# Kernel optimization log

Hardware: AMD Instinct MI355X
Metric: run time of the kernel (lower is better)

Reference implementation:

```python
import jax, jax.numpy as jnp
import numpy as np

D_MODEL = 1024
N_HEADS = 16
D_FF = 512  # FeedForward default d_ff=512 (not overridden in EncoderLayer)
EPS = 1e-6


def _norm(x, alpha, bias):
    # Custom NormLayer: mean + UNBIASED variance (torch.var default, N-1 denom)
    mean = jnp.mean(x, axis=-1, keepdims=True)
    n = x.shape[-1]
    var = jnp.sum((x - mean) ** 2, axis=-1, keepdims=True) / (n - 1)
    return alpha * (x - mean) / jnp.sqrt(var + EPS) + bias


def setup_inputs() -> dict:
    key = jax.random.key(0)
    ks = jax.random.split(key, 12)
    s = 1.0 / np.sqrt(D_MODEL)
    inp = {
        "x": jax.random.normal(ks[0], (2, 2048, D_MODEL), dtype=jnp.float32),
        "Wq": jax.random.uniform(ks[1], (D_MODEL, D_MODEL), jnp.float32, -s, s),
        "bq": jnp.zeros((D_MODEL,), jnp.float32),
        "Wk": jax.random.uniform(ks[2], (D_MODEL, D_MODEL), jnp.float32, -s, s),
        "bk": jnp.zeros((D_MODEL,), jnp.float32),
        "Wv": jax.random.uniform(ks[3], (D_MODEL, D_MODEL), jnp.float32, -s, s),
        "bv": jnp.zeros((D_MODEL,), jnp.float32),
        "Wo": jax.random.uniform(ks[4], (D_MODEL, D_MODEL), jnp.float32, -s, s),
        "bo": jnp.zeros((D_MODEL,), jnp.float32),
        "alpha1": jnp.ones((D_MODEL,), jnp.float32),
        "beta1": jnp.zeros((D_MODEL,), jnp.float32),
        "alpha2": jnp.ones((D_MODEL,), jnp.float32),
        "beta2": jnp.zeros((D_MODEL,), jnp.float32),
        "W1": jax.random.uniform(ks[5], (D_MODEL, D_FF), jnp.float32, -s, s),
        "b1": jnp.zeros((D_FF,), jnp.float32),
        "W2": jax.random.uniform(ks[6], (D_FF, D_MODEL), jnp.float32, -1.0 / np.sqrt(D_FF), 1.0 / np.sqrt(D_FF)),
        "b2": jnp.zeros((D_MODEL,), jnp.float32),
    }
    return inp


def reference(x, Wq, bq, Wk, bk, Wv, bv, Wo, bo, alpha1, beta1, alpha2, beta2, W1, b1, W2, b2):
    B, S, D = x.shape
    H = N_HEADS
    dh = D // H
    # norm_1 applied to x, result feeds BOTH attention and the residual
    x = _norm(x, alpha1, beta1)
    # multihead attention (dropout = identity in eval)
    q = (x @ Wq + bq).reshape(B, S, H, dh)
    k = (x @ Wk + bk).reshape(B, S, H, dh)
    v = (x @ Wv + bv).reshape(B, S, H, dh)
    scores = jnp.einsum("bqhd,bkhd->bhqk", q, k) / jnp.sqrt(jnp.asarray(dh, x.dtype))
    attn = jax.nn.softmax(scores, axis=-1)
    o = jnp.einsum("bhqk,bkhd->bqhd", attn, v).reshape(B, S, D)
    o = o @ Wo + bo
    x = x + o
    # FFN on norm_2(x)
    h = _norm(x, alpha2, beta2)
    h = jax.nn.relu(h @ W1 + b1) @ W2 + b2
    return x + h
```

## Files before the change

kernel.cpp:

```cpp
#include <hip/hip_runtime.h>

typedef __bf16 bf16;
typedef __bf16 bf16x4 __attribute__((ext_vector_type(4)));
typedef __bf16 bf16x8 __attribute__((ext_vector_type(8)));
typedef float f32x4 __attribute__((ext_vector_type(4)));

#define D_MODEL 1024
#define SEQ 2048
#define NB 2
#define LOG2E 1.4426950408889634f

__device__ __forceinline__ void glds16(const bf16* g, bf16* l) {
    __builtin_amdgcn_global_load_lds(
        (const __attribute__((address_space(1))) void*)g,
        (__attribute__((address_space(3))) void*)l, 16, 0, 0);
}

__device__ __forceinline__ void tile_tcvt(
    const float* __restrict__ src, int rows, int cols, bf16* __restrict__ dst,
    int bx, int by, bf16 (*t)[72])
{
    int tid = threadIdx.x;
    int k0 = by * 64, n0 = bx * 64;
    int r = tid >> 2, c = (tid & 3) * 16;
    const float4* s = (const float4*)(src + (size_t)(k0 + r) * cols + n0 + c);
#pragma unroll
    for (int q = 0; q < 4; ++q) {
        float4 v = s[q];
        t[c + q * 4 + 0][r] = (bf16)v.x;
        t[c + q * 4 + 1][r] = (bf16)v.y;
        t[c + q * 4 + 2][r] = (bf16)v.z;
        t[c + q * 4 + 3][r] = (bf16)v.w;
    }
    __syncthreads();
    bf16* d = dst + (size_t)(n0 + r) * rows + k0 + c;
    *(bf16x8*)(d)     = *(const bf16x8*)&t[r][c];
    *(bf16x8*)(d + 8) = *(const bf16x8*)&t[r][c + 8];
}

__device__ __forceinline__ void norm_row(
    const float* __restrict__ X, const float* __restrict__ alpha,
    const float* __restrict__ beta, bf16* __restrict__ Y, int row)
{
    int tid = threadIdx.x;
    float4 v = ((const float4*)(X + (size_t)row * D_MODEL))[tid];
    float s = v.x + v.y + v.z + v.w;
    float ss = v.x*v.x + v.y*v.y + v.z*v.z + v.w*v.w;
#pragma unroll
    for (int off = 1; off < 64; off <<= 1) {
        s  += __shfl_xor(s, off, 64);
        ss += __shfl_xor(ss, off, 64);
    }
    __shared__ float sd[8];
    int wave = tid >> 6, lane = tid & 63;
    if (lane == 0) { sd[wave] = s; sd[4 + wave] = ss; }
    __syncthreads();
    s  = sd[0] + sd[1] + sd[2] + sd[3];
    ss = sd[4] + sd[5] + sd[6] + sd[7];
    float mean = s * (1.0f / 1024.0f);
    float var  = (ss - s * mean) * (1.0f / 1023.0f);
    float rs = rsqrtf(var + 1e-6f);
    float4 a = ((const float4*)alpha)[tid];
    float4 bt = ((const float4*)beta)[tid];
    bf16x4 o;
    o[0] = (bf16)(a.x * (v.x - mean) * rs + bt.x);
    o[1] = (bf16)(a.y * (v.y - mean) * rs + bt.y);
    o[2] = (bf16)(a.z * (v.z - mean) * rs + bt.z);
    o[3] = (bf16)(a.w * (v.w - mean) * rs + bt.w);
    *(bf16x4*)(Y + (size_t)row * D_MODEL + tid * 4) = o;
}

__global__ __launch_bounds__(256) void prep_norm_kernel(
    const float* __restrict__ x, const float* __restrict__ alpha1,
    const float* __restrict__ beta1, bf16* __restrict__ xn,
    const float* __restrict__ Wq, const float* __restrict__ Wk,
    const float* __restrict__ Wv, const float* __restrict__ Wo,
    const float* __restrict__ W1, const float* __restrict__ W2,
    const float* __restrict__ bq, const float* __restrict__ bk,
    const float* __restrict__ bv,
    bf16* __restrict__ Wqkv_t, bf16* __restrict__ Wo_t,
    bf16* __restrict__ W1_t, bf16* __restrict__ W2_t,
    float* __restrict__ b_qkv)
{
    __shared__ bf16 t[64][72];
    int id = blockIdx.x;
    if (id < 4096) {
        norm_row(x, alpha1, beta1, xn, id);
        return;
    }
    id -= 4096;
    if (id < 1024) {
        int which = id >> 8, tile = id & 255;
        const float* src = which == 0 ? Wq : which == 1 ? Wk : which == 2 ? Wv : Wo;
        bf16* dst = which == 3 ? Wo_t : Wqkv_t + (size_t)which * 1024 * 1024;
        tile_tcvt(src, 1024, 1024, dst, tile & 15, tile >> 4, t);
    } else if (id < 1152) {
        int tile = id - 1024;
        tile_tcvt(W1, 1024, 512, W1_t, tile & 7, tile >> 3, t);
    } else if (id < 1280) {
        int tile = id - 1152;
        tile_tcvt(W2, 512, 1024, W2_t, tile & 15, tile >> 4, t);
    } else {
        int i = (id - 1280) * 256 + threadIdx.x;
        float v;
        if (i < 1024) v = bq[i];
        else if (i < 2048) v = bk[i - 1024];
        else v = bv[i - 2048];
        b_qkv[i] = v;
    }
}

__global__ __launch_bounds__(256) void norm_kernel(
    const float* __restrict__ X, const float* __restrict__ alpha,
    const float* __restrict__ beta, bf16* __restrict__ Y)
{
    norm_row(X, alpha, beta, Y, blockIdx.x);
}

__global__ __launch_bounds__(256) void crelu_kernel(
    const float* __restrict__ p0, const float* __restrict__ p1,
    const float* __restrict__ b1, bf16* __restrict__ h1)
{
    int i = blockIdx.x * 256 + threadIdx.x;
    float4 a = ((const float4*)p0)[i];
    float4 b = ((const float4*)p1)[i];
    int col = (i * 4) & 511;
    float4 bb = *(const float4*)(b1 + col);
    bf16x4 o;
    o[0] = (bf16)fmaxf(a.x + b.x + bb.x, 0.0f);
    o[1] = (bf16)fmaxf(a.y + b.y + bb.y, 0.0f);
    o[2] = (bf16)fmaxf(a.z + b.z + bb.z, 0.0f);
    o[3] = (bf16)fmaxf(a.w + b.w + bb.w, 0.0f);
    ((bf16x4*)h1)[i] = o;
}

template <typename OutT, int BN, int KU, bool VFUSE, bool SPLITK>
__global__ __launch_bounds__(256) void gemm128(
    const bf16* __restrict__ A, const bf16* __restrict__ Bt,
    const float* __restrict__ bias, const bf16* __restrict__ Rb,
    const float* __restrict__ Rf, OutT* __restrict__ C, bf16* __restrict__ vT,
    int M, int N, int K, int lda, int relu)
{
    constexpr int NT = BN / 32;
    constexpr int ASTR = 128 * 32;
    constexpr int BSTR = BN * 32;
    __shared__ bf16 As[ASTR * KU];
    __shared__ bf16 Bs[BSTR * KU];

    int tid = threadIdx.x;
    int wave = tid >> 6, lane = tid & 63;
    int quad = lane >> 4, l16 = lane & 15;
    int m0 = blockIdx.y * 128, n0 = blockIdx.x * BN;
    int wm = (wave >> 1) * 64, wn = (wave & 1) * (BN / 2);
    int Keff = SPLITK ? (K >> 1) : K;
    int klo  = SPLITK ? blockIdx.z * Keff : 0;

    f32x4 acc[4][NT] = {};

    const bf16* ga = A  + (size_t)(m0 + (tid >> 2)) * lda + (tid & 3) * 8 + klo;
    const bf16* gb = Bt + (size_t)(n0 + (tid >> 2)) * K   + (tid & 3) * 8 + klo;
    bf16* lAs = As + wave * 512;
    bf16* lBs = Bs + wave * 512;

    for (int k0 = 0; k0 < Keff; k0 += 32 * KU) {
        __syncthreads();
#pragma unroll
        for (int u = 0; u < KU; ++u) {
            glds16(ga + k0 + u * 32, lAs + u * ASTR);
            glds16(ga + (size_t)64 * lda + k0 + u * 32, lAs + u * ASTR + 2048);
            glds16(gb + k0 + u * 32, lBs + u * BSTR);
            if (BN == 128) glds16(gb + (size_t)64 * K + k0 + u * 32, lBs + u * BSTR + 2048);
        }
        __syncthreads();
#pragma unroll
        for (int u = 0; u < KU; ++u) {
            bf16x8 af[4], bfr[NT];
#pragma unroll
            for (int mt = 0; mt < 4; ++mt)
                af[mt] = *(const bf16x8*)(As + u * ASTR + (wm + mt * 16 + l16) * 32 + quad * 8);
#pragma unroll
            for (int nt = 0; nt < NT; ++nt)
                bfr[nt] = *(const bf16x8*)(Bs + u * BSTR + (wn + nt * 16 + l16) * 32 + quad * 8);
#pragma unroll
            for (int mt = 0; mt < 4; ++mt)
#pragma unroll
                for (int nt = 0; nt < NT; ++nt)
                    acc[mt][nt] = __builtin_amdgcn_mfma_f32_16x16x32_bf16(af[mt], bfr[nt], acc[mt][nt], 0, 0, 0);
        }
    }

    if (SPLITK) {
        float* P = (float*)C + (size_t)blockIdx.z * M * N;
#pragma unroll
        for (int nt = 0; nt < NT; ++nt) {
            int n = n0 + wn + nt * 16 + l16;
#pragma unroll
            for (int mt = 0; mt < 4; ++mt)
#pragma unroll
                for (int r = 0; r < 4; ++r) {
                    int m = m0 + wm + mt * 16 + quad * 4 + r;
                    P[(size_t)m * N + n] = acc[mt][nt][r];
                }
        }
        return;
    }

#pragma unroll
    for (int nt = 0; nt < NT; ++nt) {
        int n = n0 + wn + nt * 16 + l16;
        float bv = bias[n];
        if (VFUSE && n >= 2048) {
            int d = n & 63, h = (n - 2048) >> 6;
#pragma unroll
            for (int mt = 0; mt < 4; ++mt) {
                int m = m0 + wm + mt * 16 + quad * 4;
                int b = m >> 11, sidx = m & 2047;
                bf16x4 pk;
#pragma unroll
                for (int r = 0; r < 4; ++r) pk[r] = (bf16)(acc[mt][nt][r] + bv);
                *(bf16x4*)(vT + (((size_t)(b * 16 + h) * 64 + d) * SEQ + sidx)) = pk;
            }
        } else {
#pragma unroll
            for (int mt = 0; mt < 4; ++mt) {
#pragma unroll
                for (int r = 0; r < 4; ++r) {
                    int m = m0 + wm + mt * 16 + quad * 4 + r;
                    float vv = acc[mt][nt][r] + bv;
                    if (Rb) vv += (float)Rb[(size_t)m * N + n];
                    if (Rf) vv += Rf[(size_t)m * N + n];
                    if (relu) vv = vv > 0.0f ? vv : 0.0f;
                    C[(size_t)m * N + n] = (OutT)vv;
                }
            }
        }
    }
}

__global__ __launch_bounds__(512) void attn_kernel(
    const bf16* __restrict__ qkv, const bf16* __restrict__ vT, bf16* __restrict__ O)
{
    __shared__ __align__(16) char smem[38912];
    bf16* Ks = (bf16*)smem;
    bf16* Vt = (bf16*)(smem + 9216);
    bf16* Ps = (bf16*)(smem + 18432);

    int tid = threadIdx.x;
    int wave = tid >> 6, lane = tid & 63;
    int quad = lane >> 4, l16 = lane & 15;
    int qg = wave >> 1, kg = wave & 1;
    int bh = blockIdx.y, b = bh >> 4, h = bh & 15;
    int q0 = blockIdx.x * 128 + qg * 32;

    const bf16* Qb = qkv + (size_t)(b * SEQ + q0) * 3072 + h * 64;
    const bf16* Kb = qkv + (size_t)(b * SEQ) * 3072 + 1024 + h * 64;
    const bf16* Vb = vT + (size_t)bh * 64 * SEQ;

    const float c_l2 = 0.125f * LOG2E;
    bf16x8 qa[2][2];
#pragma unroll
    for (int mt = 0; mt < 2; ++mt)
#pragma unroll
        for (int hf = 0; hf < 2; ++hf) {
            bf16x8 raw = *(const bf16x8*)(Qb + (size_t)(mt * 16 + l16) * 3072 + hf * 32 + quad * 8);
            bf16x8 sc;
#pragma unroll
            for (int j = 0; j < 8; ++j) sc[j] = (bf16)((float)raw[j] * c_l2);
            qa[mt][hf] = sc;
        }

    float lsum[2] = {};
    f32x4 oacc[2][4] = {};

    int sr = tid >> 3, scol = (tid & 7) * 8;
    const bf16* kp = Kb + (size_t)sr * 3072 + scol;
    const bf16* vp = Vb + (size_t)sr * SEQ + scol;
    bf16x8 kr = *(const bf16x8*)kp;
    bf16x8 vr = *(const bf16x8*)vp;

    bf16* PsW = Ps + wave * 32 * 40;
    const bf16* KsKg = Ks + kg * 32 * 72;

    for (int kt = 0; kt < SEQ; kt += 64) {
        __syncthreads();
        *(bf16x8*)(Ks + sr * 72 + scol) = kr;
        *(bf16x8*)(Vt + sr * 72 + scol) = vr;
        __syncthreads();
        if (kt + 64 < SEQ) {
            kr = *(const bf16x8*)(kp + (size_t)(kt + 64) * 3072);
            vr = *(const bf16x8*)(vp + kt + 64);
        }

        bf16x8 kb[2][2], vb[4];
#pragma unroll
        for (int t4 = 0; t4 < 2; ++t4) {
            kb[t4][0] = *(const bf16x8*)(KsKg + (t4 * 16 + l16) * 72 + quad * 8);
            kb[t4][1] = *(const bf16x8*)(KsKg + (t4 * 16 + l16) * 72 + 32 + quad * 8);
        }
#pragma unroll
        for (int dt = 0; dt < 4; ++dt)
            vb[dt] = *(const bf16x8*)(Vt + (dt * 16 + l16) * 72 + kg * 32 + quad * 8);

#pragma unroll
        for (int mt = 0; mt < 2; ++mt)
#pragma unroll
            for (int t4 = 0; t4 < 2; ++t4) {
                f32x4 c = {};
                c = __builtin_amdgcn_mfma_f32_16x16x32_bf16(kb[t4][0], qa[mt][0], c, 0, 0, 0);
                c = __builtin_amdgcn_mfma_f32_16x16x32_bf16(kb[t4][1], qa[mt][1], c, 0, 0, 0);
                bf16x4 pk;
                float psum = 0.0f;
#pragma unroll
                for (int r = 0; r < 4; ++r) {
                    float p = exp2f(c[r]);
                    psum += p;
                    pk[r] = (bf16)p;
                }
                lsum[mt] += psum;
                *(bf16x4*)(PsW + (mt * 16 + l16) * 40 + t4 * 16 + quad * 4) = pk;
            }
#pragma unroll
        for (int mt = 0; mt < 2; ++mt) {
            bf16x8 pa = *(const bf16x8*)(PsW + (mt * 16 + l16) * 40 + quad * 8);
#pragma unroll
            for (int dt = 0; dt < 4; ++dt)
                oacc[mt][dt] = __builtin_amdgcn_mfma_f32_16x16x32_bf16(pa, vb[dt], oacc[mt][dt], 0, 0, 0);
        }
    }

    float lr[2];
#pragma unroll
    for (int mt = 0; mt < 2; ++mt) {
        lr[mt] = lsum[mt];
        lr[mt] += __shfl_xor(lr[mt], 16);
        lr[mt] += __shfl_xor(lr[mt], 32);
    }
    __syncthreads();
    float* sf = (float*)smem;
    float* lb = sf + 8192;
    if (kg == 1) {
#pragma unroll
        for (int mt = 0; mt < 2; ++mt)
#pragma unroll
            for (int dt = 0; dt < 4; ++dt)
                *(f32x4*)&sf[qg * 2048 + (dt * 16 + l16) * 32 + mt * 16 + quad * 4] = oacc[mt][dt];
        if (lane < 16) {
            lb[(qg * 2 + 0) * 16 + l16] = lr[0];
            lb[(qg * 2 + 1) * 16 + l16] = lr[1];
        }
    }
    __syncthreads();
    if (kg == 0) {
#pragma unroll
        for (int mt = 0; mt < 2; ++mt) {
            lr[mt] += lb[(qg * 2 + mt) * 16 + l16];
#pragma unroll
            for (int dt = 0; dt < 4; ++dt) {
                f32x4 other = *(const f32x4*)&sf[qg * 2048 + (dt * 16 + l16) * 32 + mt * 16 + quad * 4];
                oacc[mt][dt] += other;
            }
        }
#pragma unroll
        for (int mt = 0; mt < 2; ++mt)
#pragma unroll
            for (int r = 0; r < 4; ++r) {
                float inv = 1.0f / __shfl(lr[mt], quad * 4 + r, 16);
                int row = b * SEQ + q0 + mt * 16 + quad * 4 + r;
                bf16* op = O + (size_t)row * D_MODEL + h * 64;
#pragma unroll
                for (int dt = 0; dt < 4; ++dt)
                    op[dt * 16 + l16] = (bf16)(oacc[mt][dt][r] * inv);
            }
    }
}

extern "C" void kernel_launch(void* const* d_in, const int* in_sizes, int n_in,
                              void* d_out, int out_size, void* d_ws, size_t ws_size,
                              hipStream_t stream)
{
    const float* x      = (const float*)d_in[0];
    const float* Wq     = (const float*)d_in[1];
    const float* bq     = (const float*)d_in[2];
    const float* Wk     = (const float*)d_in[3];
    const float* bk     = (const float*)d_in[4];
    const float* Wv     = (const float*)d_in[5];
    const float* bv     = (const float*)d_in[6];
    const float* Wo     = (const float*)d_in[7];
    const float* bo     = (const float*)d_in[8];
    const float* alpha1 = (const float*)d_in[9];
    const float* beta1  = (const float*)d_in[10];
    const float* alpha2 = (const float*)d_in[11];
    const float* beta2  = (const float*)d_in[12];
    const float* W1     = (const float*)d_in[13];
    const float* b1     = (const float*)d_in[14];
    const float* W2     = (const float*)d_in[15];
    const float* b2     = (const float*)d_in[16];

    char* ws = (char*)d_ws;
    const size_t MB = 1ull << 20;
    bf16*  Wqkv_t = (bf16*)(ws + 0 * MB);
    bf16*  Wo_t   = (bf16*)(ws + 6 * MB);
    bf16*  W1_t   = (bf16*)(ws + 8 * MB);
    bf16*  W2_t   = (bf16*)(ws + 9 * MB);
    float* b_qkv  = (float*)(ws + 10 * MB);
    bf16*  xn     = (bf16*)(ws + 11 * MB);
    bf16*  qkv    = (bf16*)(ws + 19 * MB);
    bf16*  vT     = (bf16*)(ws + 43 * MB);
    bf16*  o      = (bf16*)(ws + 51 * MB);
    float* x2     = (float*)(ws + 19 * MB);
    bf16*  hn     = (bf16*)(ws + 35 * MB);
    float* pF1    = (float*)(ws + 43 * MB);
    bf16*  h1     = (bf16*)(ws + 11 * MB);

    const int M = NB * SEQ;

    prep_norm_kernel<<<4096 + 1292, 256, 0, stream>>>(
        x, alpha1, beta1, xn, Wq, Wk, Wv, Wo, W1, W2, bq, bk, bv,
        Wqkv_t, Wo_t, W1_t, W2_t, b_qkv);

    gemm128<bf16, 128, 2, true, false><<<dim3(24, 32), 256, 0, stream>>>(
        xn, Wqkv_t, b_qkv, nullptr, nullptr, qkv, vT, M, 3072, D_MODEL, D_MODEL, 0);

    attn_kernel<<<dim3(SEQ / 128, 32), 512, 0, stream>>>(qkv, vT, o);

    gemm128<float, 64, 4, false, false><<<dim3(16, 32), 256, 0, stream>>>(
        o, Wo_t, bo, xn, nullptr, x2, nullptr, M, D_MODEL, D_MODEL, D_MODEL, 0);

    norm_kernel<<<M, 256, 0, stream>>>(x2, alpha2, beta2, hn);

    gemm128<float, 64, 4, false, true><<<dim3(8, 32, 2), 256, 0, stream>>>(
        hn, W1_t, nullptr, nullptr, nullptr, pF1, nullptr, M, 512, D_MODEL, D_MODEL, 0);

    crelu_kernel<<<(M * 512) / 1024, 256, 0, stream>>>(
        pF1, pF1 + (size_t)M * 512, b1, h1);

    gemm128<float, 64, 4, false, false><<<dim3(16, 32), 256, 0, stream>>>(
        h1, W2_t, b2, nullptr, x2, (float*)d_out, nullptr, M, D_MODEL, 512, 512, 0);
}
```

Measured before the change: 270.0 us.

## Split attention over two KV halves with a separate merge kernel

Adds a split-KV mode in which each attention block processes half of the key sequence and writes unnormalized fp32 partial outputs and row sums to workspace. A new merge kernel adds the two partials and normalizes them into the bf16 output. This doubles the number of attention blocks to raise occupancy and parallelism. The cost is extra global memory traffic for the fp32 partials and one more kernel launch. The mode is enabled only when the workspace is large enough.

```diff
diff --git a/kernel.cpp b/kernel.cpp
--- a/kernel.cpp
+++ b/kernel.cpp
@@ -237,8 +237,10 @@
     }
 }
 
+template <bool SPLIT>
 __global__ __launch_bounds__(512) void attn_kernel(
-    const bf16* __restrict__ qkv, const bf16* __restrict__ vT, bf16* __restrict__ O)
+    const bf16* __restrict__ qkv, const bf16* __restrict__ vT,
+    bf16* __restrict__ O, float* __restrict__ pO, float* __restrict__ pL)
 {
     __shared__ __align__(16) char smem[38912];
     bf16* Ks = (bf16*)smem;
@@ -251,10 +253,13 @@
     int qg = wave >> 1, kg = wave & 1;
     int bh = blockIdx.y, b = bh >> 4, h = bh & 15;
     int q0 = blockIdx.x * 128 + qg * 32;
+    int z = SPLIT ? blockIdx.z : 0;
+    int kbase = SPLIT ? z * (SEQ / 2) : 0;
+    const int kend = SPLIT ? (SEQ / 2) : SEQ;
 
     const bf16* Qb = qkv + (size_t)(b * SEQ + q0) * 3072 + h * 64;
-    const bf16* Kb = qkv + (size_t)(b * SEQ) * 3072 + 1024 + h * 64;
-    const bf16* Vb = vT + (size_t)bh * 64 * SEQ;
+    const bf16* Kb = qkv + (size_t)(b * SEQ + kbase) * 3072 + 1024 + h * 64;
+    const bf16* Vb = vT + (size_t)bh * 64 * SEQ + kbase;
 
     const float c_l2 = 0.125f * LOG2E;
     bf16x8 qa[2][2];
@@ -281,12 +286,12 @@
     bf16* PsW = Ps + wave * 32 * 40;
     const bf16* KsKg = Ks + kg * 32 * 72;
 
-    for (int kt = 0; kt < SEQ; kt += 64) {
+    for (int kt = 0; kt < kend; kt += 64) {
         __syncthreads();
         *(bf16x8*)(Ks + sr * 72 + scol) = kr;
         *(bf16x8*)(Vt + sr * 72 + scol) = vr;
         __syncthreads();
-        if (kt + 64 < SEQ) {
+        if (kt + 64 < kend) {
             kr = *(const bf16x8*)(kp + (size_t)(kt + 64) * 3072);
             vr = *(const bf16x8*)(vp + kt + 64);
         }
@@ -360,18 +365,56 @@
                 oacc[mt][dt] += other;
             }
         }
-#pragma unroll
-        for (int mt = 0; mt < 2; ++mt)
-#pragma unroll
-            for (int r = 0; r < 4; ++r) {
-                float inv = 1.0f / __shfl(lr[mt], quad * 4 + r, 16);
-                int row = b * SEQ + q0 + mt * 16 + quad * 4 + r;
-                bf16* op = O + (size_t)row * D_MODEL + h * 64;
-#pragma unroll
-                for (int dt = 0; dt < 4; ++dt)
-                    op[dt * 16 + l16] = (bf16)(oacc[mt][dt][r] * inv);
+        if (!SPLIT) {
+#pragma unroll
+            for (int mt = 0; mt < 2; ++mt)
+#pragma unroll
+                for (int r = 0; r < 4; ++r) {
+                    float inv = 1.0f / __shfl(lr[mt], quad * 4 + r, 16);
+                    int row = b * SEQ + q0 + mt * 16 + quad * 4 + r;
+                    bf16* op = O + (size_t)row * D_MODEL + h * 64;
+#pragma unroll
+                    for (int dt = 0; dt < 4; ++dt)
+                        op[dt * 16 + l16] = (bf16)(oacc[mt][dt][r] * inv);
+                }
+        } else {
+            if (lane < 16) {
+#pragma unroll
+                for (int mt = 0; mt < 2; ++mt)
+                    pL[((size_t)z * 32 + bh) * SEQ + q0 + mt * 16 + lane] = lr[mt];
             }
-    }
+#pragma unroll
+            for (int mt = 0; mt < 2; ++mt)
+#pragma unroll
+                for (int r = 0; r < 4; ++r) {
+                    int row = b * SEQ + q0 + mt * 16 + quad * 4 + r;
+                    float* pp = pO + ((size_t)z * 4096 + row) * 1024 + h * 64;
+#pragma unroll
+                    for (int dt = 0; dt < 4; ++dt)
+                        pp[dt * 16 + l16] = oacc[mt][dt][r];
+                }
+        }
+    }
+}
+
+__global__ __launch_bounds__(256) void amerge_kernel(
+    const float* __restrict__ pO, const float* __restrict__ pL,
+    bf16* __restrict__ O)
+{
+    int i = blockIdx.x * 256 + threadIdx.x;
+    int row = i >> 8;
+    int col = (i & 255) * 4;
+    int b = row >> 11, q = row & 2047, h = col >> 6;
+    int bh = b * 16 + h;
+    float l0 = pL[(size_t)bh * SEQ + q];
+    float l1 = pL[(size_t)(32 + bh) * SEQ + q];
+    float inv = 1.0f / (l0 + l1);
+    f32x4 a = ((const f32x4*)pO)[i];
+    f32x4 c = ((const f32x4*)(pO + (size_t)4096 * 1024))[i];
+    bf16x4 o;
+#pragma unroll
+    for (int r = 0; r < 4; ++r) o[r] = (bf16)((a[r] + c[r]) * inv);
+    ((bf16x4*)O)[i] = o;
 }
 
 extern "C" void kernel_launch(void* const* d_in, const int* in_sizes, int n_in,
@@ -411,8 +454,11 @@
     bf16*  hn     = (bf16*)(ws + 35 * MB);
     float* pF1    = (float*)(ws + 43 * MB);
     bf16*  h1     = (bf16*)(ws + 11 * MB);
+    float* pO     = (float*)(ws + 59 * MB);
+    float* pL     = (float*)(ws + 91 * MB);
 
     const int M = NB * SEQ;
+    const bool split = ws_size >= 92 * MB;
 
     prep_norm_kernel<<<4096 + 1292, 256, 0, stream>>>(
         x, alpha1, beta1, xn, Wq, Wk, Wv, Wo, W1, W2, bq, bk, bv,
@@ -421,7 +467,14 @@
     gemm128<bf16, 128, 2, true, false><<<dim3(24, 32), 256, 0, stream>>>(
         xn, Wqkv_t, b_qkv, nullptr, nullptr, qkv, vT, M, 3072, D_MODEL, D_MODEL, 0);
 
-    attn_kernel<<<dim3(SEQ / 128, 32), 512, 0, stream>>>(qkv, vT, o);
+    if (split) {
+        attn_kernel<true><<<dim3(SEQ / 128, 32, 2), 512, 0, stream>>>(
+            qkv, vT, nullptr, pO, pL);
+        amerge_kernel<<<(M * D_MODEL) / 1024, 256, 0, stream>>>(pO, pL, o);
+    } else {
+        attn_kernel<false><<<dim3(SEQ / 128, 32), 512, 0, stream>>>(
+            qkv, vT, o, nullptr, nullptr);
+    }
 
     gemm128<float, 64, 4, false, false><<<dim3(16, 32), 256, 0, stream>>>(
         o, Wo_t, bo, xn, nullptr, x2, nullptr, M, D_MODEL, D_MODEL, D_MODEL, 0);
```

Result: slower. 277.6 us (+2.8%).

## Keep softmax probabilities in registers via permlane swaps and halve attention LDS

Applied to the files above, without the earlier changes.

The P tile is no longer round-tripped through shared memory between the QK^T and PV MFMAs. Probabilities are packed to bf16 with v_cvt_pk_bf16_f32 and rearranged into the A-operand layout using v_permlane32/16_swap. The final cross-wave reduction is split so each key-group wave reduces and writes half of the output columns, which shrinks the LDS buffer from about 38KB to 19KB and may allow more blocks per CU. The cost is an extra barrier and reduction phase, plus inline asm that depends on lane-permutation correctness.

```diff
diff --git a/kernel.cpp b/kernel.cpp
--- a/kernel.cpp
+++ b/kernel.cpp
@@ -4,6 +4,7 @@
 typedef __bf16 bf16x4 __attribute__((ext_vector_type(4)));
 typedef __bf16 bf16x8 __attribute__((ext_vector_type(8)));
 typedef float f32x4 __attribute__((ext_vector_type(4)));
+typedef unsigned u32x4 __attribute__((ext_vector_type(4)));
 
 #define D_MODEL 1024
 #define SEQ 2048
@@ -240,10 +241,9 @@
 __global__ __launch_bounds__(512) void attn_kernel(
     const bf16* __restrict__ qkv, const bf16* __restrict__ vT, bf16* __restrict__ O)
 {
-    __shared__ __align__(16) char smem[38912];
+    __shared__ __align__(16) char smem[19456];
     bf16* Ks = (bf16*)smem;
     bf16* Vt = (bf16*)(smem + 9216);
-    bf16* Ps = (bf16*)(smem + 18432);
 
     int tid = threadIdx.x;
     int wave = tid >> 6, lane = tid & 63;
@@ -251,6 +251,7 @@
     int qg = wave >> 1, kg = wave & 1;
     int bh = blockIdx.y, b = bh >> 4, h = bh & 15;
     int q0 = blockIdx.x * 128 + qg * 32;
+    const bool oddq = (lane & 16) != 0;
 
     const bf16* Qb = qkv + (size_t)(b * SEQ + q0) * 3072 + h * 64;
     const bf16* Kb = qkv + (size_t)(b * SEQ) * 3072 + 1024 + h * 64;
@@ -278,7 +279,6 @@
     bf16x8 kr = *(const bf16x8*)kp;
     bf16x8 vr = *(const bf16x8*)vp;
 
-    bf16* PsW = Ps + wave * 32 * 40;
     const bf16* KsKg = Ks + kg * 32 * 72;
 
     for (int kt = 0; kt < SEQ; kt += 64) {
@@ -302,26 +302,36 @@
             vb[dt] = *(const bf16x8*)(Vt + (dt * 16 + l16) * 72 + kg * 32 + quad * 8);
 
 #pragma unroll
-        for (int mt = 0; mt < 2; ++mt)
+        for (int mt = 0; mt < 2; ++mt) {
+            unsigned Aw[2], Bw[2];
 #pragma unroll
             for (int t4 = 0; t4 < 2; ++t4) {
                 f32x4 c = {};
                 c = __builtin_amdgcn_mfma_f32_16x16x32_bf16(kb[t4][0], qa[mt][0], c, 0, 0, 0);
                 c = __builtin_amdgcn_mfma_f32_16x16x32_bf16(kb[t4][1], qa[mt][1], c, 0, 0, 0);
-                bf16x4 pk;
-                float psum = 0.0f;
-#pragma unroll
-                for (int r = 0; r < 4; ++r) {
-                    float p = exp2f(c[r]);
-                    psum += p;
-                    pk[r] = (bf16)p;
-                }
-                lsum[mt] += psum;
-                *(bf16x4*)(PsW + (mt * 16 + l16) * 40 + t4 * 16 + quad * 4) = pk;
+                float p0 = exp2f(c[0]);
+                float p1 = exp2f(c[1]);
+                float p2 = exp2f(c[2]);
+                float p3 = exp2f(c[3]);
+                lsum[mt] += (p0 + p1) + (p2 + p3);
+                asm("v_cvt_pk_bf16_f32 %0, %1, %2" : "=v"(Aw[t4]) : "v"(p0), "v"(p1));
+                asm("v_cvt_pk_bf16_f32 %0, %1, %2" : "=v"(Bw[t4]) : "v"(p2), "v"(p3));
             }
-#pragma unroll
-        for (int mt = 0; mt < 2; ++mt) {
-            bf16x8 pa = *(const bf16x8*)(PsW + (mt * 16 + l16) * 40 + quad * 8);
+            unsigned A0 = Aw[0], A1 = Aw[1], B0 = Bw[0], B1 = Bw[1];
+            asm("v_permlane32_swap_b32 %0, %1" : "+v"(A1), "+v"(A0));
+            asm("v_permlane32_swap_b32 %0, %1" : "+v"(B1), "+v"(B0));
+            unsigned uA = A1, tA = A1, pA = A0, qA = A0;
+            asm("v_permlane16_swap_b32 %0, %1" : "+v"(tA), "+v"(uA));
+            asm("v_permlane16_swap_b32 %0, %1" : "+v"(pA), "+v"(qA));
+            unsigned uB = B1, tB = B1, pB = B0, qB = B0;
+            asm("v_permlane16_swap_b32 %0, %1" : "+v"(tB), "+v"(uB));
+            asm("v_permlane16_swap_b32 %0, %1" : "+v"(pB), "+v"(qB));
+            unsigned w0 = oddq ? uA : A0;
+            unsigned w1 = oddq ? uB : B0;
+            unsigned w2 = oddq ? A1 : pA;
+            unsigned w3 = oddq ? B1 : pB;
+            u32x4 pw = {w0, w1, w2, w3};
+            bf16x8 pa = __builtin_bit_cast(bf16x8, pw);
 #pragma unroll
             for (int dt = 0; dt < 4; ++dt)
                 oacc[mt][dt] = __builtin_amdgcn_mfma_f32_16x16x32_bf16(pa, vb[dt], oacc[mt][dt], 0, 0, 0);
@@ -337,29 +347,32 @@
     }
     __syncthreads();
     float* sf = (float*)smem;
-    float* lb = sf + 8192;
+    float* lb = (float*)(smem + 18432);
+    if (lane < 16) {
+        lb[((kg * 4 + qg) * 2 + 0) * 16 + l16] = lr[0];
+        lb[((kg * 4 + qg) * 2 + 1) * 16 + l16] = lr[1];
+    }
     if (kg == 1) {
 #pragma unroll
         for (int mt = 0; mt < 2; ++mt)
 #pragma unroll
-            for (int dt = 0; dt < 4; ++dt)
-                *(f32x4*)&sf[qg * 2048 + (dt * 16 + l16) * 32 + mt * 16 + quad * 4] = oacc[mt][dt];
-        if (lane < 16) {
-            lb[(qg * 2 + 0) * 16 + l16] = lr[0];
-            lb[(qg * 2 + 1) * 16 + l16] = lr[1];
-        }
+            for (int dt = 0; dt < 2; ++dt)
+                *(f32x4*)&sf[((qg * 2 + dt) * 16 + l16) * 36 + mt * 16 + quad * 4] = oacc[mt][dt];
     }
     __syncthreads();
     if (kg == 0) {
 #pragma unroll
         for (int mt = 0; mt < 2; ++mt) {
-            lr[mt] += lb[(qg * 2 + mt) * 16 + l16];
-#pragma unroll
-            for (int dt = 0; dt < 4; ++dt) {
-                f32x4 other = *(const f32x4*)&sf[qg * 2048 + (dt * 16 + l16) * 32 + mt * 16 + quad * 4];
-                oacc[mt][dt] += other;
-            }
-        }
+            lr[mt] += lb[((4 + qg) * 2 + mt) * 16 + l16];
+#pragma unroll
+            for (int dt = 0; dt < 2; ++dt)
+                oacc[mt][dt] += *(const f32x4*)&sf[((qg * 2 + dt) * 16 + l16) * 36 + mt * 16 + quad * 4];
+        }
+#pragma unroll
+        for (int mt = 0; mt < 2; ++mt)
+#pragma unroll
+            for (int dt = 0; dt < 2; ++dt)
+                *(f32x4*)&sf[((qg * 2 + dt) * 16 + l16) * 36 + mt * 16 + quad * 4] = oacc[mt][dt + 2];
 #pragma unroll
         for (int mt = 0; mt < 2; ++mt)
 #pragma unroll
@@ -367,9 +380,28 @@
                 float inv = 1.0f / __shfl(lr[mt], quad * 4 + r, 16);
                 int row = b * SEQ + q0 + mt * 16 + quad * 4 + r;
                 bf16* op = O + (size_t)row * D_MODEL + h * 64;
-#pragma unroll
-                for (int dt = 0; dt < 4; ++dt)
-                    op[dt * 16 + l16] = (bf16)(oacc[mt][dt][r] * inv);
+                op[l16]      = (bf16)(oacc[mt][0][r] * inv);
+                op[16 + l16] = (bf16)(oacc[mt][1][r] * inv);
+            }
+    }
+    __syncthreads();
+    if (kg == 1) {
+#pragma unroll
+        for (int mt = 0; mt < 2; ++mt) {
+            lr[mt] += lb[(qg * 2 + mt) * 16 + l16];
+#pragma unroll
+            for (int dt = 0; dt < 2; ++dt)
+                oacc[mt][dt + 2] += *(const f32x4*)&sf[((qg * 2 + dt) * 16 + l16) * 36 + mt * 16 + quad * 4];
+        }
+#pragma unroll
+        for (int mt = 0; mt < 2; ++mt)
+#pragma unroll
+            for (int r = 0; r < 4; ++r) {
+                float inv = 1.0f / __shfl(lr[mt], quad * 4 + r, 16);
+                int row = b * SEQ + q0 + mt * 16 + quad * 4 + r;
+                bf16* op = O + (size_t)row * D_MODEL + h * 64;
+                op[32 + l16] = (bf16)(oacc[mt][2][r] * inv);
+                op[48 + l16] = (bf16)(oacc[mt][3][r] * inv);
             }
     }
 }
```

Result: slower. 288.0 us (+6.6%).
